# Kernel tuning notes

Measured on AMD Instinct MI355X. Metric: run time of the kernel, lower is better.

The kernel has to match this reference:

```python
import math
import jax, jax.numpy as jnp
import numpy as np

DIM = 256
B, S = 4, 4096

def setup_inputs() -> dict:
    key = jax.random.key(0)
    k1, k2, k3, k4 = jax.random.split(key, 4)
    x = jax.random.normal(k1, (B, S, DIM), dtype=jnp.float32)
    W = jax.random.normal(k2, (3 * DIM, DIM), dtype=jnp.float32) * 0.02
    b = jax.random.normal(k3, (3 * DIM,), dtype=jnp.float32) * 0.02
    attention_mask = jax.random.randint(k4, (B, 1, S), 0, 2, dtype=jnp.int32)
    return {"x": x, "W": W, "b": b, "attention_mask": attention_mask}

def reference(x, W, b, attention_mask):
    # qkv projection: Linear(dim, 3*dim) -> x @ W^T + b
    qkv = jnp.einsum("bsd,ed->bse", x, W) + b  # [B,S,3*DIM]
    q, k, v = jnp.split(qkv, 3, axis=-1)
    # NOTE: module computes q @ v^T (not q @ k^T) -- faithful to source
    scores = jnp.einsum("bqd,bkd->bqk", q, v) / math.sqrt(DIM)  # [B,S,S]
    scores = jnp.where(attention_mask == 0, -jnp.inf, scores)
    attn = jax.nn.softmax(scores, axis=-1)
    # dropout in eval mode -> identity
    out = jnp.einsum("bqk,bkd->bqd", attn, v)  # [B,S,DIM]
    return out
```

## Files before the change

kernel.cpp:

```cpp
#include <hip/hip_runtime.h>
#include <hip/hip_bf16.h>

#define DIMC 256
#define NB 4
#define NS 4096
#define KT 64
#define VS_ELEMS (KT * DIMC)

typedef __attribute__((ext_vector_type(4))) float f32x4;
typedef __attribute__((ext_vector_type(8))) short bf16x8;

__device__ __forceinline__ ushort f2bf(float f) {
  __hip_bfloat16 h = __float2bfloat16(f);
  return *reinterpret_cast<ushort*>(&h);
}
__device__ __forceinline__ float bf2f(ushort h) {
  uint u = ((uint)h) << 16;
  float f;
  __builtin_memcpy(&f, &u, 4);
  return f;
}

__device__ __forceinline__ void gload16(const ushort* g, ushort* l) {
  __builtin_amdgcn_global_load_lds(
      (const __attribute__((address_space(1))) unsigned int*)g,
      (__attribute__((address_space(3))) unsigned int*)l,
      16, 0, 0);
}

__global__ void wsplit_kernel(const float* __restrict__ W, ushort* __restrict__ Whl) {
  const int col = blockIdx.x;
  const int k = threadIdx.x;
  const int srcrow = (col < 256) ? col : (col + 256);
  float f = W[(size_t)srcrow * 256 + k];
  ushort h = f2bf(f);
  Whl[(size_t)col * 256 + k] = h;
  Whl[131072 + (size_t)col * 256 + k] = f2bf(f - bf2f(h));
}

__global__ __launch_bounds__(256) void qv_proj_kernel(
    const float* __restrict__ x, const ushort* __restrict__ Whl,
    const float* __restrict__ bias,
    ushort* __restrict__ qb, ushort* __restrict__ vb, ushort* __restrict__ vtb)
{
  const int tid  = threadIdx.x;
  const int w    = tid >> 6;
  const int lane = tid & 63;
  const int l15  = lane & 15;
  const int g    = (lane >> 4) & 3;
  const int r0   = blockIdx.x << 6;
  const int colbase = w << 7;

  __shared__ ushort olds[64 * 520];

  f32x4 acc[4][8];
  #pragma unroll
  for (int rt = 0; rt < 4; ++rt)
    #pragma unroll
    for (int ct = 0; ct < 8; ++ct) { acc[rt][ct].x=0.f; acc[rt][ct].y=0.f; acc[rt][ct].z=0.f; acc[rt][ct].w=0.f; }

  #pragma unroll 1
  for (int st = 0; st < 8; ++st) {
    bf16x8 xh[4], xl[4];
    #pragma unroll
    for (int rt = 0; rt < 4; ++rt) {
      const float* p = x + (size_t)(r0 + rt * 16 + l15) * DIMC + st * 32 + g * 8;
      float4 f0 = *(const float4*)p;
      float4 f1 = *(const float4*)(p + 4);
      union { bf16x8 v; ushort u[8]; } uh, ul;
      #pragma unroll
      for (int e = 0; e < 8; ++e) {
        float fe = (e < 4) ? ((const float*)&f0)[e] : ((const float*)&f1)[e - 4];
        ushort h = f2bf(fe);
        uh.u[e] = h;
        ul.u[e] = f2bf(fe - bf2f(h));
      }
      xh[rt] = uh.v;
      xl[rt] = ul.v;
    }
    #pragma unroll
    for (int ct = 0; ct < 8; ++ct) {
      const ushort* wp = Whl + (size_t)(colbase + ct * 16 + l15) * 256 + st * 32 + g * 8;
      bf16x8 wh = *(const bf16x8*)wp;
      bf16x8 wl = *(const bf16x8*)(wp + 131072);
      #pragma unroll
      for (int rt = 0; rt < 4; ++rt) {
        acc[rt][ct] = __builtin_amdgcn_mfma_f32_16x16x32_bf16(xh[rt], wh, acc[rt][ct], 0, 0, 0);
        acc[rt][ct] = __builtin_amdgcn_mfma_f32_16x16x32_bf16(xl[rt], wh, acc[rt][ct], 0, 0, 0);
        acc[rt][ct] = __builtin_amdgcn_mfma_f32_16x16x32_bf16(xh[rt], wl, acc[rt][ct], 0, 0, 0);
      }
    }
  }

  const float qscale = (colbase < 256) ? 0.0625f : 1.0f;
  #pragma unroll
  for (int ct = 0; ct < 8; ++ct) {
    const int col = colbase + ct * 16 + l15;
    const float bv = bias[(col < 256) ? col : (col + 256)];
    #pragma unroll
    for (int rt = 0; rt < 4; ++rt) {
      #pragma unroll
      for (int r = 0; r < 4; ++r)
        olds[(rt * 16 + 4 * g + r) * 520 + col] = f2bf((acc[rt][ct][r] + bv) * qscale);
    }
  }
  __syncthreads();

  #pragma unroll
  for (int i = 0; i < 16; ++i) {
    int task = tid + i * 256;
    int row = task >> 6, ch = task & 63;
    uint4 d = *(const uint4*)&olds[row * 520 + ch * 8];
    if (ch < 32) *(uint4*)&qb[(size_t)(r0 + row) * DIMC + ch * 8] = d;
    else         *(uint4*)&vb[(size_t)(r0 + row) * DIMC + (ch - 32) * 8] = d;
  }
  const int bbp = r0 >> 12;
  const int s0  = r0 & (NS - 1);
  const int vcol = tid;
  #pragma unroll
  for (int o = 0; o < 8; ++o) {
    union { uint4 v; ushort u[8]; } pk;
    #pragma unroll
    for (int j = 0; j < 8; ++j)
      pk.u[j] = olds[(o * 8 + j) * 520 + 256 + vcol];
    *(uint4*)&vtb[((size_t)(bbp * DIMC + vcol)) * NS + s0 + o * 8] = pk.v;
  }
}

__global__ void mask_pack_kernel(const int* __restrict__ mask, uint* __restrict__ pm32) {
  int t = blockIdx.x * 64 + threadIdx.x;
  int b = t >> 7;
  int kt = (t >> 1) & 63;
  int kh = t & 1;
  const int* mrow = mask + b * NS + kt * 64 + kh * 32;
  uint wd = 0;
  for (int g = 0; g < 4; ++g)
    for (int ntl = 0; ntl < 2; ++ntl)
      for (int r = 0; r < 4; ++r)
        if (mrow[ntl * 16 + 4 * g + r] != 0) wd |= 1u << (8 * g + ntl * 4 + r);
  pm32[t] = wd;
}

__global__ __launch_bounds__(512, 1) void attn_kernel(
    const ushort* __restrict__ qb, const ushort* __restrict__ vb,
    const ushort* __restrict__ vtb, const uint* __restrict__ pm32,
    float* __restrict__ outA, float* __restrict__ opB,
    float* __restrict__ mlA, float* __restrict__ mlB)
{
  const int tid  = threadIdx.x;
  const int w    = tid >> 6;
  const int lane = tid & 63;
  const int l15  = lane & 15;
  const int g    = (lane >> 4) & 3;
  const int kh   = w & 1;
  const int pq   = w >> 1;

  const int s     = blockIdx.x & 1;
  const int qb128 = blockIdx.x >> 1;
  const int qrow0 = qb128 << 7;
  const int bb    = qrow0 >> 12;
  const int koff  = s << 11;

  float* opart = s ? opB : outA;
  float* mlp   = s ? mlB : mlA;

  extern __shared__ __align__(16) char smem[];
  uint*   pmlds = (uint*)smem;
  ushort* vs0  = (ushort*)(smem + 1024);
  ushort* vs1  = vs0 + VS_ELEMS;
  ushort* vt0  = vs1 + VS_ELEMS;
  ushort* vt1  = vt0 + VS_ELEMS;
  ushort* psb  = vt1 + VS_ELEMS;

  bf16x8 qreg[2][8];
  #pragma unroll
  for (int qt = 0; qt < 2; ++qt) {
    const int qrow = qrow0 + (pq << 5) + (qt << 4) + l15;
    #pragma unroll
    for (int st = 0; st < 8; ++st)
      qreg[qt][st] = *(const bf16x8*)&qb[(size_t)qrow * DIMC + ((st * 4 + g) << 3)];
  }

  if (tid < 128) pmlds[tid] = pm32[(bb << 7) + tid];

  auto stage = [&](int kt, ushort* vsN, ushort* vtN) {
    const ushort* vbase = vb + ((size_t)(bb * NS + koff + kt * KT)) * DIMC;
    #pragma unroll
    for (int i = 0; i < 4; ++i) {
      int rr0 = (w << 3) + (i << 1);
      int row = rr0 + (lane >> 5);
      int cs  = lane & 31;
      gload16(vbase + row * DIMC + ((cs ^ (row & 7)) << 3), vsN + (rr0 << 8));
    }
    #pragma unroll
    for (int i = 0; i < 4; ++i) {
      int d0 = i << 6;
      int dim = (d0 + lane) ^ ((w & 3) << 1);
      gload16(vtb + ((size_t)(bb * DIMC + dim)) * NS + koff + kt * KT + (w << 3),
              vtN + ((w << 8) + d0) * 8);
    }
  };

  stage(0, vs0, vt0);
  __syncthreads();

  f32x4 acc_o[2][8];
  #pragma unroll
  for (int qt = 0; qt < 2; ++qt)
    #pragma unroll
    for (int nt = 0; nt < 8; ++nt) { acc_o[qt][nt].x=0.f; acc_o[qt][nt].y=0.f; acc_o[qt][nt].z=0.f; acc_o[qt][nt].w=0.f; }
  float l_s[2] = {0.f, 0.f};

  ushort* psw = psb + pq * (32 * 72);

  auto tile_body = [&](int kt, const ushort* vs_, const ushort* vt_,
                       ushort* vsN, ushort* vtN) {
    if (kt + 1 < 32) stage(kt + 1, vsN, vtN);

    f32x4 sacc[2][2];
    #pragma unroll
    for (int qt = 0; qt < 2; ++qt) {
      sacc[qt][0].x=0.f; sacc[qt][0].y=0.f; sacc[qt][0].z=0.f; sacc[qt][0].w=0.f;
      sacc[qt][1] = sacc[qt][0];
    }
    __builtin_amdgcn_s_setprio(1);
    #pragma unroll
    for (int st = 0; st < 8; ++st) {
      const int key0 = (kh << 5) + l15;
      bf16x8 af0 = *(const bf16x8*)&vs_[(key0 * 32 + ((st * 4 + g) ^ (key0 & 7))) * 8];
      const int key1 = key0 + 16;
      bf16x8 af1 = *(const bf16x8*)&vs_[(key1 * 32 + ((st * 4 + g) ^ (key1 & 7))) * 8];
      #pragma unroll
      for (int qt = 0; qt < 2; ++qt) {
        sacc[qt][0] = __builtin_amdgcn_mfma_f32_16x16x32_bf16(af0, qreg[qt][st], sacc[qt][0], 0, 0, 0);
        sacc[qt][1] = __builtin_amdgcn_mfma_f32_16x16x32_bf16(af1, qreg[qt][st], sacc[qt][1], 0, 0, 0);
      }
    }
    __builtin_amdgcn_s_setprio(0);

    const int ktg = (s << 5) + kt;
    uint mybits = (pmlds[(ktg << 1) + kh] >> (g << 3)) & 0xffu;

    #pragma unroll
    for (int qt = 0; qt < 2; ++qt) {
      float p[8];
      #pragma unroll
      for (int ntl = 0; ntl < 2; ++ntl)
        #pragma unroll
        for (int r = 0; r < 4; ++r) {
          float vv = (mybits & (1u << (ntl * 4 + r))) ? sacc[qt][ntl][r] : -1e30f;
          p[ntl * 4 + r] = __expf(vv);
        }
      float rs = ((p[0] + p[1]) + (p[2] + p[3])) + ((p[4] + p[5]) + (p[6] + p[7]));
      rs += __shfl_xor(rs, 16);
      rs += __shfl_xor(rs, 32);
      l_s[qt] += rs;
      #pragma unroll
      for (int ntl = 0; ntl < 2; ++ntl) {
        uint2 pk;
        pk.x = (uint)f2bf(p[ntl*4+0]) | ((uint)f2bf(p[ntl*4+1]) << 16);
        pk.y = (uint)f2bf(p[ntl*4+2]) | ((uint)f2bf(p[ntl*4+3]) << 16);
        *(uint2*)&psw[((qt << 4) + l15) * 72 + (kh << 5) + ntl * 16 + 4 * g] = pk;
      }
    }

    asm volatile("s_waitcnt lgkmcnt(0)" ::: "memory");
    __builtin_amdgcn_sched_barrier(0);
    __builtin_amdgcn_s_barrier();
    __builtin_amdgcn_sched_barrier(0);

    bf16x8 pa[2][2];
    #pragma unroll
    for (int qt = 0; qt < 2; ++qt)
      #pragma unroll
      for (int ks2 = 0; ks2 < 2; ++ks2)
        pa[qt][ks2] = *(const bf16x8*)&psw[((qt << 4) + l15) * 72 + (ks2 << 5) + (g << 3)];
    __builtin_amdgcn_s_setprio(1);
    #pragma unroll
    for (int ntl = 0; ntl < 8; ++ntl) {
      const int d = ((kh << 3) + ntl) * 16 + l15;
      #pragma unroll
      for (int ks2 = 0; ks2 < 2; ++ks2) {
        const int kc = (ks2 << 2) + g;
        bf16x8 vf = *(const bf16x8*)&vt_[((kc << 8) + (d ^ ((kc & 3) << 1))) * 8];
        acc_o[0][ntl] = __builtin_amdgcn_mfma_f32_16x16x32_bf16(vf, pa[0][ks2], acc_o[0][ntl], 0, 0, 0);
        acc_o[1][ntl] = __builtin_amdgcn_mfma_f32_16x16x32_bf16(vf, pa[1][ks2], acc_o[1][ntl], 0, 0, 0);
      }
    }
    __builtin_amdgcn_s_setprio(0);

    __syncthreads();
  };

  for (int kt2 = 0; kt2 < 32; kt2 += 2) {
    tile_body(kt2,     vs0, vt0, vs1, vt1);
    tile_body(kt2 + 1, vs1, vt1, vs0, vt0);
  }

  #pragma unroll
  for (int qt = 0; qt < 2; ++qt) {
    const int qrow = qrow0 + (pq << 5) + (qt << 4) + l15;
    const size_t obase = (size_t)qrow * DIMC + 4 * g;
    #pragma unroll
    for (int ntl = 0; ntl < 8; ++ntl) {
      f32x4 o = acc_o[qt][ntl];
      *(float4*)&opart[obase + ((kh << 3) + ntl) * 16] = *(float4*)&o;
    }
    if (g == 0) mlp[(size_t)qrow * 2 + kh] = l_s[qt];
  }
}

__global__ __launch_bounds__(256) void merge_kernel(
    float* __restrict__ outA, const float* __restrict__ opB,
    const float* __restrict__ mlA, const float* __restrict__ mlB)
{
  int id = blockIdx.x * 256 + threadIdx.x;
  int row = id >> 6;
  int c = (id & 63) << 2;
  float lT = (mlA[(size_t)row * 2] + mlA[(size_t)row * 2 + 1]) +
             (mlB[(size_t)row * 2] + mlB[(size_t)row * 2 + 1]);
  float inv = 1.f / lT;
  size_t o = (size_t)row * DIMC + c;
  float4 a = *(const float4*)&outA[o];
  float4 b = *(const float4*)&opB[o];
  float4 r;
  r.x = (a.x + b.x) * inv;
  r.y = (a.y + b.y) * inv;
  r.z = (a.z + b.z) * inv;
  r.w = (a.w + b.w) * inv;
  *(float4*)&outA[o] = r;
}

extern "C" void kernel_launch(void* const* d_in, const int* in_sizes, int n_in,
                              void* d_out, int out_size, void* d_ws, size_t ws_size,
                              hipStream_t stream) {
  const float* x    = (const float*)d_in[0];
  const float* W    = (const float*)d_in[1];
  const float* bias = (const float*)d_in[2];
  const int*   mask = (const int*)d_in[3];
  float* out = (float*)d_out;

  const size_t n = (size_t)NB * NS * DIMC;
  ushort* qb  = (ushort*)d_ws;
  ushort* vb  = qb + n;
  ushort* vtb = vb + n;
  uint* pm32 = (uint*)(vtb + n);
  ushort* Whl = (ushort*)(pm32 + 512);
  float* opB = (float*)(Whl + 262144);
  float* mlA = opB + n;
  float* mlB = mlA + 2 * (NB * NS);

  wsplit_kernel<<<512, 256, 0, stream>>>(W, Whl);
  mask_pack_kernel<<<8, 64, 0, stream>>>(mask, pm32);
  qv_proj_kernel<<<(NB * NS) / 64, 256, 0, stream>>>(x, Whl, bias, qb, vb, vtb);

  const int smem_bytes = 1024 + 4 * VS_ELEMS * 2 + 4 * 32 * 72 * 2;
  attn_kernel<<<256, 512, smem_bytes, stream>>>(qb, vb, vtb, pm32, out, opB, mlA, mlB);
  merge_kernel<<<(NB * NS * DIMC / 4) / 256, 256, 0, stream>>>(out, opB, mlA, mlB);
}
```

Before: 173.3 us.

## Software-pipeline attention PV with next QK tile and merge prep kernels

The attention loop is restructured so each iteration computes the QK^T scores for tile t while doing the P·V MFMAs for tile t-1. The V^T tile is now staged one step later, and the waits use explicit vmcnt counts instead of a full __syncthreads, which lets global loads and the two matmul phases overlap and removes one barrier's worth of stall per tile. The W split and mask pack kernels are also merged into one launch to save a kernel launch. In exchange there is more register pressure from holding the probabilities across the barrier, and a hand-counted vmcnt that must match the number of outstanding loads.

```diff
diff --git a/kernel.cpp b/kernel.cpp
--- a/kernel.cpp
+++ b/kernel.cpp
@@ -28,14 +28,31 @@
       16, 0, 0);
 }
 
-__global__ void wsplit_kernel(const float* __restrict__ W, ushort* __restrict__ Whl) {
-  const int col = blockIdx.x;
-  const int k = threadIdx.x;
-  const int srcrow = (col < 256) ? col : (col + 256);
-  float f = W[(size_t)srcrow * 256 + k];
-  ushort h = f2bf(f);
-  Whl[(size_t)col * 256 + k] = h;
-  Whl[131072 + (size_t)col * 256 + k] = f2bf(f - bf2f(h));
+__global__ __launch_bounds__(256) void prep_kernel(
+    const float* __restrict__ W, const int* __restrict__ mask,
+    ushort* __restrict__ Whl, uint* __restrict__ pm32)
+{
+  if (blockIdx.x < 512) {
+    const int col = blockIdx.x;
+    const int k = threadIdx.x;
+    const int srcrow = (col < 256) ? col : (col + 256);
+    float f = W[(size_t)srcrow * 256 + k];
+    ushort h = f2bf(f);
+    Whl[(size_t)col * 256 + k] = h;
+    Whl[131072 + (size_t)col * 256 + k] = f2bf(f - bf2f(h));
+  } else {
+    int t = (blockIdx.x - 512) * 256 + threadIdx.x;
+    int b = t >> 7;
+    int kt = (t >> 1) & 63;
+    int kh = t & 1;
+    const int* mrow = mask + b * NS + kt * 64 + kh * 32;
+    uint wd = 0;
+    for (int g = 0; g < 4; ++g)
+      for (int ntl = 0; ntl < 2; ++ntl)
+        for (int r = 0; r < 4; ++r)
+          if (mrow[ntl * 16 + 4 * g + r] != 0) wd |= 1u << (8 * g + ntl * 4 + r);
+    pm32[t] = wd;
+  }
 }
 
 __global__ __launch_bounds__(256) void qv_proj_kernel(
@@ -125,20 +142,6 @@
       pk.u[j] = olds[(o * 8 + j) * 520 + 256 + vcol];
     *(uint4*)&vtb[((size_t)(bbp * DIMC + vcol)) * NS + s0 + o * 8] = pk.v;
   }
-}
-
-__global__ void mask_pack_kernel(const int* __restrict__ mask, uint* __restrict__ pm32) {
-  int t = blockIdx.x * 64 + threadIdx.x;
-  int b = t >> 7;
-  int kt = (t >> 1) & 63;
-  int kh = t & 1;
-  const int* mrow = mask + b * NS + kt * 64 + kh * 32;
-  uint wd = 0;
-  for (int g = 0; g < 4; ++g)
-    for (int ntl = 0; ntl < 2; ++ntl)
-      for (int r = 0; r < 4; ++r)
-        if (mrow[ntl * 16 + 4 * g + r] != 0) wd |= 1u << (8 * g + ntl * 4 + r);
-  pm32[t] = wd;
 }
 
 __global__ __launch_bounds__(512, 1) void attn_kernel(
@@ -183,7 +186,7 @@
 
   if (tid < 128) pmlds[tid] = pm32[(bb << 7) + tid];
 
-  auto stage = [&](int kt, ushort* vsN, ushort* vtN) {
+  auto stage_vs = [&](int kt, ushort* vsN) {
     const ushort* vbase = vb + ((size_t)(bb * NS + koff + kt * KT)) * DIMC;
     #pragma unroll
     for (int i = 0; i < 4; ++i) {
@@ -192,6 +195,8 @@
       int cs  = lane & 31;
       gload16(vbase + row * DIMC + ((cs ^ (row & 7)) << 3), vsN + (rr0 << 8));
     }
+  };
+  auto stage_vt = [&](int kt, ushort* vtN) {
     #pragma unroll
     for (int i = 0; i < 4; ++i) {
       int d0 = i << 6;
@@ -201,7 +206,7 @@
     }
   };
 
-  stage(0, vs0, vt0);
+  stage_vs(0, vs0);
   __syncthreads();
 
   f32x4 acc_o[2][8];
@@ -213,9 +218,15 @@
 
   ushort* psw = psb + pq * (32 * 72);
 
-  auto tile_body = [&](int kt, const ushort* vs_, const ushort* vt_,
-                       ushort* vsN, ushort* vtN) {
-    if (kt + 1 < 32) stage(kt + 1, vsN, vtN);
+  #pragma unroll 1
+  for (int t = 0; t < 32; ++t) {
+    ushort* vsQ = (t & 1) ? vs1 : vs0;
+    ushort* vsS = (t & 1) ? vs0 : vs1;
+    ushort* vtS = (t & 1) ? vt1 : vt0;
+    ushort* vtP = (t & 1) ? vt0 : vt1;
+
+    if (t + 1 < 32) stage_vs(t + 1, vsS);
+    stage_vt(t, vtS);
 
     f32x4 sacc[2][2];
     #pragma unroll
@@ -227,9 +238,9 @@
     #pragma unroll
     for (int st = 0; st < 8; ++st) {
       const int key0 = (kh << 5) + l15;
-      bf16x8 af0 = *(const bf16x8*)&vs_[(key0 * 32 + ((st * 4 + g) ^ (key0 & 7))) * 8];
+      bf16x8 af0 = *(const bf16x8*)&vsQ[(key0 * 32 + ((st * 4 + g) ^ (key0 & 7))) * 8];
       const int key1 = key0 + 16;
-      bf16x8 af1 = *(const bf16x8*)&vs_[(key1 * 32 + ((st * 4 + g) ^ (key1 & 7))) * 8];
+      bf16x8 af1 = *(const bf16x8*)&vsQ[(key1 * 32 + ((st * 4 + g) ^ (key1 & 7))) * 8];
       #pragma unroll
       for (int qt = 0; qt < 2; ++qt) {
         sacc[qt][0] = __builtin_amdgcn_mfma_f32_16x16x32_bf16(af0, qreg[qt][st], sacc[qt][0], 0, 0, 0);
@@ -238,30 +249,45 @@
     }
     __builtin_amdgcn_s_setprio(0);
 
-    const int ktg = (s << 5) + kt;
+    if (t > 0) {
+      bf16x8 pa[2][2];
+      #pragma unroll
+      for (int qt = 0; qt < 2; ++qt)
+        #pragma unroll
+        for (int ks2 = 0; ks2 < 2; ++ks2)
+          pa[qt][ks2] = *(const bf16x8*)&psw[((qt << 4) + l15) * 72 + (ks2 << 5) + (g << 3)];
+      __builtin_amdgcn_s_setprio(1);
+      #pragma unroll
+      for (int ntl = 0; ntl < 8; ++ntl) {
+        const int d = ((kh << 3) + ntl) * 16 + l15;
+        #pragma unroll
+        for (int ks2 = 0; ks2 < 2; ++ks2) {
+          const int kc = (ks2 << 2) + g;
+          bf16x8 vf = *(const bf16x8*)&vtP[((kc << 8) + (d ^ ((kc & 3) << 1))) * 8];
+          acc_o[0][ntl] = __builtin_amdgcn_mfma_f32_16x16x32_bf16(vf, pa[0][ks2], acc_o[0][ntl], 0, 0, 0);
+          acc_o[1][ntl] = __builtin_amdgcn_mfma_f32_16x16x32_bf16(vf, pa[1][ks2], acc_o[1][ntl], 0, 0, 0);
+        }
+      }
+      __builtin_amdgcn_s_setprio(0);
+    }
+
+    const int ktg = (s << 5) + t;
     uint mybits = (pmlds[(ktg << 1) + kh] >> (g << 3)) & 0xffu;
-
+    float pv[2][8];
     #pragma unroll
     for (int qt = 0; qt < 2; ++qt) {
-      float p[8];
       #pragma unroll
       for (int ntl = 0; ntl < 2; ++ntl)
         #pragma unroll
         for (int r = 0; r < 4; ++r) {
           float vv = (mybits & (1u << (ntl * 4 + r))) ? sacc[qt][ntl][r] : -1e30f;
-          p[ntl * 4 + r] = __expf(vv);
+          pv[qt][ntl * 4 + r] = __expf(vv);
         }
-      float rs = ((p[0] + p[1]) + (p[2] + p[3])) + ((p[4] + p[5]) + (p[6] + p[7]));
+      float rs = ((pv[qt][0] + pv[qt][1]) + (pv[qt][2] + pv[qt][3])) +
+                 ((pv[qt][4] + pv[qt][5]) + (pv[qt][6] + pv[qt][7]));
       rs += __shfl_xor(rs, 16);
       rs += __shfl_xor(rs, 32);
       l_s[qt] += rs;
-      #pragma unroll
-      for (int ntl = 0; ntl < 2; ++ntl) {
-        uint2 pk;
-        pk.x = (uint)f2bf(p[ntl*4+0]) | ((uint)f2bf(p[ntl*4+1]) << 16);
-        pk.y = (uint)f2bf(p[ntl*4+2]) | ((uint)f2bf(p[ntl*4+3]) << 16);
-        *(uint2*)&psw[((qt << 4) + l15) * 72 + (kh << 5) + ntl * 16 + 4 * g] = pk;
-      }
     }
 
     asm volatile("s_waitcnt lgkmcnt(0)" ::: "memory");
@@ -269,6 +295,32 @@
     __builtin_amdgcn_s_barrier();
     __builtin_amdgcn_sched_barrier(0);
 
+    #pragma unroll
+    for (int qt = 0; qt < 2; ++qt) {
+      #pragma unroll
+      for (int ntl = 0; ntl < 2; ++ntl) {
+        uint2 pk;
+        pk.x = (uint)f2bf(pv[qt][ntl*4+0]) | ((uint)f2bf(pv[qt][ntl*4+1]) << 16);
+        pk.y = (uint)f2bf(pv[qt][ntl*4+2]) | ((uint)f2bf(pv[qt][ntl*4+3]) << 16);
+        *(uint2*)&psw[((qt << 4) + l15) * 72 + (kh << 5) + ntl * 16 + 4 * g] = pk;
+      }
+    }
+
+    if (t + 1 < 32)
+      asm volatile("s_waitcnt vmcnt(8) lgkmcnt(0)" ::: "memory");
+    else
+      asm volatile("s_waitcnt vmcnt(4) lgkmcnt(0)" ::: "memory");
+    __builtin_amdgcn_sched_barrier(0);
+    __builtin_amdgcn_s_barrier();
+    __builtin_amdgcn_sched_barrier(0);
+  }
+
+  asm volatile("s_waitcnt vmcnt(0)" ::: "memory");
+  __builtin_amdgcn_sched_barrier(0);
+  __builtin_amdgcn_s_barrier();
+  __builtin_amdgcn_sched_barrier(0);
+  {
+    ushort* vtP = vt1;
     bf16x8 pa[2][2];
     #pragma unroll
     for (int qt = 0; qt < 2; ++qt)
@@ -282,19 +334,12 @@
       #pragma unroll
       for (int ks2 = 0; ks2 < 2; ++ks2) {
         const int kc = (ks2 << 2) + g;
-        bf16x8 vf = *(const bf16x8*)&vt_[((kc << 8) + (d ^ ((kc & 3) << 1))) * 8];
+        bf16x8 vf = *(const bf16x8*)&vtP[((kc << 8) + (d ^ ((kc & 3) << 1))) * 8];
         acc_o[0][ntl] = __builtin_amdgcn_mfma_f32_16x16x32_bf16(vf, pa[0][ks2], acc_o[0][ntl], 0, 0, 0);
         acc_o[1][ntl] = __builtin_amdgcn_mfma_f32_16x16x32_bf16(vf, pa[1][ks2], acc_o[1][ntl], 0, 0, 0);
       }
     }
     __builtin_amdgcn_s_setprio(0);
-
-    __syncthreads();
-  };
-
-  for (int kt2 = 0; kt2 < 32; kt2 += 2) {
-    tile_body(kt2,     vs0, vt0, vs1, vt1);
-    tile_body(kt2 + 1, vs1, vt1, vs0, vt0);
   }
 
   #pragma unroll
@@ -350,8 +395,7 @@
   float* mlA = opB + n;
   float* mlB = mlA + 2 * (NB * NS);
 
-  wsplit_kernel<<<512, 256, 0, stream>>>(W, Whl);
-  mask_pack_kernel<<<8, 64, 0, stream>>>(mask, pm32);
+  prep_kernel<<<514, 256, 0, stream>>>(W, mask, Whl, pm32);
   qv_proj_kernel<<<(NB * NS) / 64, 256, 0, stream>>>(x, Whl, bias, qb, vb, vtb);
 
   const int smem_bytes = 1024 + 4 * VS_ELEMS * 2 + 4 * 32 * 72 * 2;
```

New measurement: 147.8 us. -14.7%, faster.

## Keep softmax probabilities in registers by permuting V-transpose layout, split keys per wave

Applied to the files above, without the earlier changes.

The V-transpose written by the projection kernel is reordered so that the bf16 probability fragments from the QV MFMA can feed the PV MFMA directly from registers. This removes the LDS round trip for P and one barrier per tile. Each key-half wave now accumulates all 256 output columns, which doubles the accumulator registers, and the two halves are reduced through shared memory at the end. The weight-split and mask-pack kernels are merged into one launch. The per-tile wait now covers all outstanding global loads (vmcnt(0)), which may reduce overlap of the prefetch with compute.

```diff
diff --git a/kernel.cpp b/kernel.cpp
--- a/kernel.cpp
+++ b/kernel.cpp
@@ -28,14 +28,31 @@
       16, 0, 0);
 }
 
-__global__ void wsplit_kernel(const float* __restrict__ W, ushort* __restrict__ Whl) {
-  const int col = blockIdx.x;
-  const int k = threadIdx.x;
-  const int srcrow = (col < 256) ? col : (col + 256);
-  float f = W[(size_t)srcrow * 256 + k];
-  ushort h = f2bf(f);
-  Whl[(size_t)col * 256 + k] = h;
-  Whl[131072 + (size_t)col * 256 + k] = f2bf(f - bf2f(h));
+__global__ __launch_bounds__(256) void prep_kernel(
+    const float* __restrict__ W, const int* __restrict__ mask,
+    ushort* __restrict__ Whl, uint* __restrict__ pm32)
+{
+  if (blockIdx.x < 512) {
+    const int col = blockIdx.x;
+    const int k = threadIdx.x;
+    const int srcrow = (col < 256) ? col : (col + 256);
+    float f = W[(size_t)srcrow * 256 + k];
+    ushort h = f2bf(f);
+    Whl[(size_t)col * 256 + k] = h;
+    Whl[131072 + (size_t)col * 256 + k] = f2bf(f - bf2f(h));
+  } else {
+    int t = (blockIdx.x - 512) * 256 + threadIdx.x;
+    int b = t >> 7;
+    int kt = (t >> 1) & 63;
+    int kh = t & 1;
+    const int* mrow = mask + b * NS + kt * 64 + kh * 32;
+    uint wd = 0;
+    for (int g = 0; g < 4; ++g)
+      for (int ntl = 0; ntl < 2; ++ntl)
+        for (int r = 0; r < 4; ++r)
+          if (mrow[ntl * 16 + 4 * g + r] != 0) wd |= 1u << (8 * g + ntl * 4 + r);
+    pm32[t] = wd;
+  }
 }
 
 __global__ __launch_bounds__(256) void qv_proj_kernel(
@@ -121,24 +138,12 @@
   for (int o = 0; o < 8; ++o) {
     union { uint4 v; ushort u[8]; } pk;
     #pragma unroll
-    for (int j = 0; j < 8; ++j)
-      pk.u[j] = olds[(o * 8 + j) * 520 + 256 + vcol];
+    for (int e = 0; e < 8; ++e) {
+      int srcrow = 32 * (o >> 2) + ((e >> 2) << 4) + ((o & 3) << 2) + (e & 3);
+      pk.u[e] = olds[srcrow * 520 + 256 + vcol];
+    }
     *(uint4*)&vtb[((size_t)(bbp * DIMC + vcol)) * NS + s0 + o * 8] = pk.v;
   }
-}
-
-__global__ void mask_pack_kernel(const int* __restrict__ mask, uint* __restrict__ pm32) {
-  int t = blockIdx.x * 64 + threadIdx.x;
-  int b = t >> 7;
-  int kt = (t >> 1) & 63;
-  int kh = t & 1;
-  const int* mrow = mask + b * NS + kt * 64 + kh * 32;
-  uint wd = 0;
-  for (int g = 0; g < 4; ++g)
-    for (int ntl = 0; ntl < 2; ++ntl)
-      for (int r = 0; r < 4; ++r)
-        if (mrow[ntl * 16 + 4 * g + r] != 0) wd |= 1u << (8 * g + ntl * 4 + r);
-  pm32[t] = wd;
 }
 
 __global__ __launch_bounds__(512, 1) void attn_kernel(
@@ -170,7 +175,6 @@
   ushort* vs1  = vs0 + VS_ELEMS;
   ushort* vt0  = vs1 + VS_ELEMS;
   ushort* vt1  = vt0 + VS_ELEMS;
-  ushort* psb  = vt1 + VS_ELEMS;
 
   bf16x8 qreg[2][8];
   #pragma unroll
@@ -183,7 +187,7 @@
 
   if (tid < 128) pmlds[tid] = pm32[(bb << 7) + tid];
 
-  auto stage = [&](int kt, ushort* vsN, ushort* vtN) {
+  auto stage_vs = [&](int kt, ushort* vsN) {
     const ushort* vbase = vb + ((size_t)(bb * NS + koff + kt * KT)) * DIMC;
     #pragma unroll
     for (int i = 0; i < 4; ++i) {
@@ -192,6 +196,8 @@
       int cs  = lane & 31;
       gload16(vbase + row * DIMC + ((cs ^ (row & 7)) << 3), vsN + (rr0 << 8));
     }
+  };
+  auto stage_vt = [&](int kt, ushort* vtN) {
     #pragma unroll
     for (int i = 0; i < 4; ++i) {
       int d0 = i << 6;
@@ -201,21 +207,28 @@
     }
   };
 
-  stage(0, vs0, vt0);
+  stage_vs(0, vs0);
+  stage_vt(0, vt0);
+  asm volatile("s_waitcnt vmcnt(0)" ::: "memory");
   __syncthreads();
 
-  f32x4 acc_o[2][8];
+  f32x4 acc_o[2][16];
   #pragma unroll
   for (int qt = 0; qt < 2; ++qt)
     #pragma unroll
-    for (int nt = 0; nt < 8; ++nt) { acc_o[qt][nt].x=0.f; acc_o[qt][nt].y=0.f; acc_o[qt][nt].z=0.f; acc_o[qt][nt].w=0.f; }
+    for (int nt = 0; nt < 16; ++nt) { acc_o[qt][nt].x=0.f; acc_o[qt][nt].y=0.f; acc_o[qt][nt].z=0.f; acc_o[qt][nt].w=0.f; }
   float l_s[2] = {0.f, 0.f};
 
-  ushort* psw = psb + pq * (32 * 72);
-
-  auto tile_body = [&](int kt, const ushort* vs_, const ushort* vt_,
-                       ushort* vsN, ushort* vtN) {
-    if (kt + 1 < 32) stage(kt + 1, vsN, vtN);
+  const int kc = (kh << 2) + g;
+
+  #pragma unroll 1
+  for (int t = 0; t < 32; ++t) {
+    ushort* vsQ = (t & 1) ? vs1 : vs0;
+    ushort* vtP = (t & 1) ? vt1 : vt0;
+    ushort* vsS = (t & 1) ? vs0 : vs1;
+    ushort* vtS = (t & 1) ? vt0 : vt1;
+
+    if (t + 1 < 32) { stage_vs(t + 1, vsS); stage_vt(t + 1, vtS); }
 
     f32x4 sacc[2][2];
     #pragma unroll
@@ -227,9 +240,9 @@
     #pragma unroll
     for (int st = 0; st < 8; ++st) {
       const int key0 = (kh << 5) + l15;
-      bf16x8 af0 = *(const bf16x8*)&vs_[(key0 * 32 + ((st * 4 + g) ^ (key0 & 7))) * 8];
+      bf16x8 af0 = *(const bf16x8*)&vsQ[(key0 * 32 + ((st * 4 + g) ^ (key0 & 7))) * 8];
       const int key1 = key0 + 16;
-      bf16x8 af1 = *(const bf16x8*)&vs_[(key1 * 32 + ((st * 4 + g) ^ (key1 & 7))) * 8];
+      bf16x8 af1 = *(const bf16x8*)&vsQ[(key1 * 32 + ((st * 4 + g) ^ (key1 & 7))) * 8];
       #pragma unroll
       for (int qt = 0; qt < 2; ++qt) {
         sacc[qt][0] = __builtin_amdgcn_mfma_f32_16x16x32_bf16(af0, qreg[qt][st], sacc[qt][0], 0, 0, 0);
@@ -238,75 +251,69 @@
     }
     __builtin_amdgcn_s_setprio(0);
 
-    const int ktg = (s << 5) + kt;
+    const int ktg = (s << 5) + t;
     uint mybits = (pmlds[(ktg << 1) + kh] >> (g << 3)) & 0xffu;
-
+    bf16x8 paq[2];
     #pragma unroll
     for (int qt = 0; qt < 2; ++qt) {
       float p[8];
       #pragma unroll
-      for (int ntl = 0; ntl < 2; ++ntl)
-        #pragma unroll
-        for (int r = 0; r < 4; ++r) {
-          float vv = (mybits & (1u << (ntl * 4 + r))) ? sacc[qt][ntl][r] : -1e30f;
-          p[ntl * 4 + r] = __expf(vv);
-        }
+      for (int e = 0; e < 8; ++e) {
+        float vv = (mybits & (1u << e)) ? sacc[qt][e >> 2][e & 3] : -1e30f;
+        p[e] = __expf(vv);
+      }
       float rs = ((p[0] + p[1]) + (p[2] + p[3])) + ((p[4] + p[5]) + (p[6] + p[7]));
       rs += __shfl_xor(rs, 16);
       rs += __shfl_xor(rs, 32);
       l_s[qt] += rs;
-      #pragma unroll
-      for (int ntl = 0; ntl < 2; ++ntl) {
-        uint2 pk;
-        pk.x = (uint)f2bf(p[ntl*4+0]) | ((uint)f2bf(p[ntl*4+1]) << 16);
-        pk.y = (uint)f2bf(p[ntl*4+2]) | ((uint)f2bf(p[ntl*4+3]) << 16);
-        *(uint2*)&psw[((qt << 4) + l15) * 72 + (kh << 5) + ntl * 16 + 4 * g] = pk;
-      }
-    }
-
-    asm volatile("s_waitcnt lgkmcnt(0)" ::: "memory");
+      union { bf16x8 v; ushort u[8]; } pk;
+      #pragma unroll
+      for (int e = 0; e < 8; ++e) pk.u[e] = f2bf(p[e]);
+      paq[qt] = pk.v;
+    }
+
+    __builtin_amdgcn_s_setprio(1);
+    #pragma unroll
+    for (int nt = 0; nt < 16; ++nt) {
+      const int d = nt * 16 + l15;
+      bf16x8 vf = *(const bf16x8*)&vtP[((kc << 8) + (d ^ (g << 1))) * 8];
+      acc_o[0][nt] = __builtin_amdgcn_mfma_f32_16x16x32_bf16(vf, paq[0], acc_o[0][nt], 0, 0, 0);
+      acc_o[1][nt] = __builtin_amdgcn_mfma_f32_16x16x32_bf16(vf, paq[1], acc_o[1][nt], 0, 0, 0);
+    }
+    __builtin_amdgcn_s_setprio(0);
+
+    asm volatile("s_waitcnt vmcnt(0) lgkmcnt(0)" ::: "memory");
     __builtin_amdgcn_sched_barrier(0);
     __builtin_amdgcn_s_barrier();
     __builtin_amdgcn_sched_barrier(0);
-
-    bf16x8 pa[2][2];
-    #pragma unroll
-    for (int qt = 0; qt < 2; ++qt)
-      #pragma unroll
-      for (int ks2 = 0; ks2 < 2; ++ks2)
-        pa[qt][ks2] = *(const bf16x8*)&psw[((qt << 4) + l15) * 72 + (ks2 << 5) + (g << 3)];
-    __builtin_amdgcn_s_setprio(1);
-    #pragma unroll
-    for (int ntl = 0; ntl < 8; ++ntl) {
-      const int d = ((kh << 3) + ntl) * 16 + l15;
-      #pragma unroll
-      for (int ks2 = 0; ks2 < 2; ++ks2) {
-        const int kc = (ks2 << 2) + g;
-        bf16x8 vf = *(const bf16x8*)&vt_[((kc << 8) + (d ^ ((kc & 3) << 1))) * 8];
-        acc_o[0][ntl] = __builtin_amdgcn_mfma_f32_16x16x32_bf16(vf, pa[0][ks2], acc_o[0][ntl], 0, 0, 0);
-        acc_o[1][ntl] = __builtin_amdgcn_mfma_f32_16x16x32_bf16(vf, pa[1][ks2], acc_o[1][ntl], 0, 0, 0);
-      }
-    }
-    __builtin_amdgcn_s_setprio(0);
-
-    __syncthreads();
-  };
-
-  for (int kt2 = 0; kt2 < 32; kt2 += 2) {
-    tile_body(kt2,     vs0, vt0, vs1, vt1);
-    tile_body(kt2 + 1, vs1, vt1, vs0, vt0);
-  }
-
-  #pragma unroll
-  for (int qt = 0; qt < 2; ++qt) {
-    const int qrow = qrow0 + (pq << 5) + (qt << 4) + l15;
-    const size_t obase = (size_t)qrow * DIMC + 4 * g;
-    #pragma unroll
-    for (int ntl = 0; ntl < 8; ++ntl) {
-      f32x4 o = acc_o[qt][ntl];
-      *(float4*)&opart[obase + ((kh << 3) + ntl) * 16] = *(float4*)&o;
-    }
-    if (g == 0) mlp[(size_t)qrow * 2 + kh] = l_s[qt];
+  }
+
+  f32x4* accS = (f32x4*)(smem + 1024);
+  float*  mlS = (float*)(smem + 1024 + 131072);
+  if (kh) {
+    #pragma unroll
+    for (int qt = 0; qt < 2; ++qt) {
+      #pragma unroll
+      for (int nt = 0; nt < 16; ++nt)
+        accS[((((pq << 1) + qt) << 6) + lane) * 16 + (nt ^ l15)] = acc_o[qt][nt];
+      if (g == 0) mlS[(((pq << 1) + qt) << 4) + l15] = l_s[qt];
+    }
+  }
+  __syncthreads();
+  if (!kh) {
+    #pragma unroll
+    for (int qt = 0; qt < 2; ++qt) {
+      float lsum = l_s[qt] + mlS[(((pq << 1) + qt) << 4) + l15];
+      const int qrow = qrow0 + (pq << 5) + (qt << 4) + l15;
+      const size_t obase = (size_t)qrow * DIMC + 4 * g;
+      #pragma unroll
+      for (int nt = 0; nt < 16; ++nt) {
+        f32x4 oB = accS[((((pq << 1) + qt) << 6) + lane) * 16 + (nt ^ l15)];
+        f32x4 o = acc_o[qt][nt] + oB;
+        *(float4*)&opart[obase + nt * 16] = *(float4*)&o;
+      }
+      if (g == 0) mlp[qrow] = lsum;
+    }
   }
 }
 
@@ -317,9 +324,7 @@
   int id = blockIdx.x * 256 + threadIdx.x;
   int row = id >> 6;
   int c = (id & 63) << 2;
-  float lT = (mlA[(size_t)row * 2] + mlA[(size_t)row * 2 + 1]) +
-             (mlB[(size_t)row * 2] + mlB[(size_t)row * 2 + 1]);
-  float inv = 1.f / lT;
+  float inv = 1.f / (mlA[row] + mlB[row]);
   size_t o = (size_t)row * DIMC + c;
   float4 a = *(const float4*)&outA[o];
   float4 b = *(const float4*)&opB[o];
@@ -348,13 +353,12 @@
   ushort* Whl = (ushort*)(pm32 + 512);
   float* opB = (float*)(Whl + 262144);
   float* mlA = opB + n;
-  float* mlB = mlA + 2 * (NB * NS);
-
-  wsplit_kernel<<<512, 256, 0, stream>>>(W, Whl);
-  mask_pack_kernel<<<8, 64, 0, stream>>>(mask, pm32);
+  float* mlB = mlA + (NB * NS);
+
+  prep_kernel<<<514, 256, 0, stream>>>(W, mask, Whl, pm32);
   qv_proj_kernel<<<(NB * NS) / 64, 256, 0, stream>>>(x, Whl, bias, qb, vb, vtb);
 
-  const int smem_bytes = 1024 + 4 * VS_ELEMS * 2 + 4 * 32 * 72 * 2;
+  const int smem_bytes = 1024 + 4 * VS_ELEMS * 2 + 512;
   attn_kernel<<<256, 512, smem_bytes, stream>>>(qb, vb, vtb, pm32, out, opB, mlA, mlB);
   merge_kernel<<<(NB * NS * DIMC / 4) / 256, 256, 0, stream>>>(out, opB, mlA, mlB);
 }
```

New measurement: 212.0 us. 22.4% more time.
